# Kernel tuning notes

Hardware: AMD Instinct MI355X
Metric: run time of the kernel (lower is better)

## Reference

```python
import jax, jax.numpy as jnp
import numpy as np

B, S, D = 16, 4096, 64

def setup_inputs() -> dict:
    key = jax.random.key(0)
    kq, kk, kv = jax.random.split(key, 3)
    Q = jax.random.normal(kq, (B, S, D), dtype=jnp.float32)
    K = jax.random.normal(kk, (B, S, D), dtype=jnp.float32)
    V = jax.random.normal(kv, (B, S, D), dtype=jnp.float32)
    return {"Q": Q, "K": K, "V": V}

def reference(Q, K, V):
    d = K.shape[2]  # feature dim, matches K.transpose(1,2).size(1) in torch
    scale = 1.0 / jnp.sqrt(jnp.asarray(d, dtype=Q.dtype))
    # scores: [B, Sq, Sk]
    scores = jnp.einsum('bqd,bkd->bqk', Q, K) * scale
    attn = jax.nn.softmax(scores, axis=-1)
    # out: [B, Sq, Dv]
    return jnp.einsum('bqk,bkd->bqd', attn, V)
```

## Files before the change

kernel.cpp:

```cpp
#include <hip/hip_runtime.h>
#include <cstdint>


#define S_LEN 4096
#define HD    64
#define NSTG  64

typedef __bf16 bf16x8 __attribute__((ext_vector_type(8)));
typedef float  f32x16 __attribute__((ext_vector_type(16)));
typedef float  f32x2  __attribute__((ext_vector_type(2)));

__device__ __forceinline__ unsigned pack_bf16(float x, float y) {
  unsigned ux = __builtin_bit_cast(unsigned, x) + 0x8000u;
  unsigned uy = __builtin_bit_cast(unsigned, y) + 0x8000u;
  return (ux >> 16) | (uy & 0xffff0000u);
}
__device__ __forceinline__ unsigned cvt_pk(float lo, float hi) {
  unsigned d;
  asm("v_cvt_pk_bf16_f32 %0, %1, %2" : "=v"(d) : "v"(lo), "v"(hi));
  return d;
}
#define AS1 __attribute__((address_space(1)))
#define AS3 __attribute__((address_space(3)))
__device__ __forceinline__ void gld16(const void* g, void* l) {
  __builtin_amdgcn_global_load_lds((const AS1 void*)(uintptr_t)g,
                                   (AS3 void*)(uintptr_t)l, 16, 0, 0);
}

__global__ __launch_bounds__(256) void prep(const float* __restrict__ K,
                                            const float* __restrict__ V,
                                            uint16_t* __restrict__ Kw,
                                            uint16_t* __restrict__ Vw) {
  if (blockIdx.x < 2048) {
    const int t   = blockIdx.x * 256 + threadIdx.x;
    const int row = t >> 3;
    const int gs  = t & 7;
    const float* p = K + (size_t)row * 64 + ((gs ^ (row & 7)) << 3);
    float4 a = *(const float4*)p;
    float4 b = *(const float4*)(p + 4);
    uint4 o = {pack_bf16(a.x, a.y), pack_bf16(a.z, a.w),
               pack_bf16(b.x, b.y), pack_bf16(b.z, b.w)};
    *(uint4*)(Kw + (size_t)t * 8) = o;
    return;
  }
  const int blk = blockIdx.x - 2048;
  const int b = blk >> 6, st = blk & 63;
  const int t = threadIdx.x;
  __shared__ uint16_t Vb[64 * 72];
  const float* src = V + ((size_t)b * S_LEN + st * 64) * 64;
  const int k = t >> 2, dq = (t & 3) * 16;
  const float* p = src + k * 64 + dq;
  float4 x0 = *(const float4*)p,       x1 = *(const float4*)(p + 4);
  float4 x2 = *(const float4*)(p + 8), x3 = *(const float4*)(p + 12);
  unsigned* dst = (unsigned*)&Vb[k * 72 + dq];
  dst[0] = pack_bf16(x0.x, x0.y); dst[1] = pack_bf16(x0.z, x0.w);
  dst[2] = pack_bf16(x1.x, x1.y); dst[3] = pack_bf16(x1.z, x1.w);
  dst[4] = pack_bf16(x2.x, x2.y); dst[5] = pack_bf16(x2.z, x2.w);
  dst[6] = pack_bf16(x3.x, x3.y); dst[7] = pack_bf16(x3.z, x3.w);
  __syncthreads();
  uint16_t* out = Vw + ((size_t)b * 64 + st) * 4096;
#pragma unroll
  for (int j = 0; j < 2; ++j) {
    const int gi = t + j * 256;
    const int d = gi >> 3, gs = gi & 7;
    const int gsx = gs ^ (d & 7);
    const int kb = ((gsx >> 1) << 4) | ((gsx & 1) << 2);
    unsigned v0 = Vb[(kb + 0) * 72 + d], v1 = Vb[(kb + 1) * 72 + d];
    unsigned v2 = Vb[(kb + 2) * 72 + d], v3 = Vb[(kb + 3) * 72 + d];
    unsigned v4 = Vb[(kb + 8) * 72 + d], v5 = Vb[(kb + 9) * 72 + d];
    unsigned v6 = Vb[(kb + 10) * 72 + d], v7 = Vb[(kb + 11) * 72 + d];
    uint4 o = {v0 | (v1 << 16), v2 | (v3 << 16), v4 | (v5 << 16), v6 | (v7 << 16)};
    *(uint4*)(out + (size_t)gi * 8) = o;
  }
}

__global__ __launch_bounds__(256, 2) void attn_fwd(
    const float* __restrict__ Qg, float* __restrict__ Og,
    const uint16_t* __restrict__ Kw, const uint16_t* __restrict__ Vw) {
  const int bid   = blockIdx.x;
  const int batch = ((bid & 7) << 1) | (bid >> 8);
  const int q0    = ((bid >> 3) & 31) << 7;

  const int tid = threadIdx.x, wave = tid >> 6, lane = tid & 63;
  const int l32 = lane & 31, h = lane >> 5;
  const int wq = wave & 1, wk = wave >> 1;

  __shared__ __align__(16) unsigned char sm[32768];

  const uint16_t* Kb  = Kw + (size_t)batch * (S_LEN * HD);
  const uint16_t* Vtb = Vw + (size_t)batch * (S_LEN * HD);

  const float cs = 0.18033688011112042f;
  bf16x8 qf[2][4];
#pragma unroll
  for (int t = 0; t < 2; ++t) {
    const int qrow = q0 + t * 64 + wq * 32 + l32;
    const float* qp = Qg + ((size_t)batch * S_LEN + qrow) * 64;
#pragma unroll
    for (int dc = 0; dc < 4; ++dc) {
      const float* p = qp + dc * 16 + h * 8;
      float4 a = *(const float4*)p;
      float4 b = *(const float4*)(p + 4);
      uint4 uu = {pack_bf16(a.x * cs, a.y * cs), pack_bf16(a.z * cs, a.w * cs),
                  pack_bf16(b.x * cs, b.y * cs), pack_bf16(b.z * cs, b.w * cs)};
      qf[t][dc] = __builtin_bit_cast(bf16x8, uu);
    }
  }

  const int sw = l32 & 7;
  int aK[4], aV[4];
#pragma unroll
  for (int dc = 0; dc < 4; ++dc)
    aK[dc] = (wk * 32 + l32) * 128 + (((dc * 2 + h) ^ sw) << 4);
#pragma unroll
  for (int kc = 0; kc < 2; ++kc) {
    aV[kc * 2 + 0] = 16384 + l32 * 128 + (((wk * 4 + kc * 2 + h) ^ sw) << 4);
    aV[kc * 2 + 1] = 16384 + (32 + l32) * 128 + (((wk * 4 + kc * 2 + h) ^ sw) << 4);
  }

  auto stage = [&](int nxt, int nb) {
    const uint16_t* ks = Kb + (size_t)nxt * 4096 + wave * 1024 + lane * 8;
    const uint16_t* vs = Vtb + (size_t)nxt * 4096 + wave * 1024 + lane * 8;
    char* kd = (char*)sm + nb * 8192 + wave * 2048;
    char* vd = (char*)sm + 16384 + nb * 8192 + wave * 2048;
    gld16(ks, kd);
    gld16(ks + 512, kd + 1024);
    gld16(vs, vd);
    gld16(vs + 512, vd + 1024);
  };
  stage(0, 0);

  float zf;
  asm("v_mov_b32 %0, 0" : "=v"(zf));
  const f32x16 z16 = {zf, zf, zf, zf, zf, zf, zf, zf,
                      zf, zf, zf, zf, zf, zf, zf, zf};

  f32x16 acc00{}, acc01{}, acc10{}, acc11{};
  f32x2 rs0{}, rs1{};

  auto body = [&](int s, int cb) {
    __syncthreads();
    if (s + 1 < NSTG) stage(s + 1, cb ^ 1);
    const char* smc = (const char*)sm;
    f32x16 sc0, sc1;
    __builtin_amdgcn_s_setprio(1);
    {
      bf16x8 ka = *(const bf16x8*)(smc + cb * 8192 + aK[0]);
      sc0 = __builtin_amdgcn_mfma_f32_32x32x16_bf16(ka, qf[0][0], z16, 0, 0, 0);
      sc1 = __builtin_amdgcn_mfma_f32_32x32x16_bf16(ka, qf[1][0], z16, 0, 0, 0);
    }
#pragma unroll
    for (int dc = 1; dc < 4; ++dc) {
      bf16x8 ka = *(const bf16x8*)(smc + cb * 8192 + aK[dc]);
      sc0 = __builtin_amdgcn_mfma_f32_32x32x16_bf16(ka, qf[0][dc], sc0, 0, 0, 0);
      sc1 = __builtin_amdgcn_mfma_f32_32x32x16_bf16(ka, qf[1][dc], sc1, 0, 0, 0);
    }
    __builtin_amdgcn_s_setprio(0);
    bf16x8 v00 = *(const bf16x8*)(smc + cb * 8192 + aV[0]);
    bf16x8 v01 = *(const bf16x8*)(smc + cb * 8192 + aV[1]);
    bf16x8 v10 = *(const bf16x8*)(smc + cb * 8192 + aV[2]);
    bf16x8 v11 = *(const bf16x8*)(smc + cb * 8192 + aV[3]);
    unsigned w0[8];
#pragma unroll
    for (int j = 0; j < 8; ++j) {
      float a0 = __builtin_amdgcn_exp2f(sc0[2 * j]);
      float a1 = __builtin_amdgcn_exp2f(sc0[2 * j + 1]);
      f32x2 ta = {a0, a1};
      rs0 += ta;
      w0[j] = cvt_pk(a0, a1);
    }
    uint4 u00 = {w0[0], w0[1], w0[2], w0[3]};
    uint4 u01 = {w0[4], w0[5], w0[6], w0[7]};
    bf16x8 pa00 = __builtin_bit_cast(bf16x8, u00);
    bf16x8 pa01 = __builtin_bit_cast(bf16x8, u01);
    __builtin_amdgcn_s_setprio(1);
    acc00 = __builtin_amdgcn_mfma_f32_32x32x16_bf16(pa00, v00, acc00, 0, 0, 0);
    acc01 = __builtin_amdgcn_mfma_f32_32x32x16_bf16(pa00, v01, acc01, 0, 0, 0);
    acc00 = __builtin_amdgcn_mfma_f32_32x32x16_bf16(pa01, v10, acc00, 0, 0, 0);
    acc01 = __builtin_amdgcn_mfma_f32_32x32x16_bf16(pa01, v11, acc01, 0, 0, 0);
    __builtin_amdgcn_s_setprio(0);
    unsigned w1[8];
#pragma unroll
    for (int j = 0; j < 8; ++j) {
      float b0 = __builtin_amdgcn_exp2f(sc1[2 * j]);
      float b1 = __builtin_amdgcn_exp2f(sc1[2 * j + 1]);
      f32x2 tb = {b0, b1};
      rs1 += tb;
      w1[j] = cvt_pk(b0, b1);
    }
    uint4 u10 = {w1[0], w1[1], w1[2], w1[3]};
    uint4 u11 = {w1[4], w1[5], w1[6], w1[7]};
    bf16x8 pa10 = __builtin_bit_cast(bf16x8, u10);
    bf16x8 pa11 = __builtin_bit_cast(bf16x8, u11);
    __builtin_amdgcn_s_setprio(1);
    acc10 = __builtin_amdgcn_mfma_f32_32x32x16_bf16(pa10, v00, acc10, 0, 0, 0);
    acc11 = __builtin_amdgcn_mfma_f32_32x32x16_bf16(pa10, v01, acc11, 0, 0, 0);
    acc10 = __builtin_amdgcn_mfma_f32_32x32x16_bf16(pa11, v10, acc10, 0, 0, 0);
    acc11 = __builtin_amdgcn_mfma_f32_32x32x16_bf16(pa11, v11, acc11, 0, 0, 0);
    __builtin_amdgcn_s_setprio(0);
  };
  for (int it = 0; it < NSTG; it += 2) { body(it, 0); body(it + 1, 1); }

  float rsum0 = rs0[0] + rs0[1];
  float rsum1 = rs1[0] + rs1[1];
  rsum0 += __shfl_xor(rsum0, 32, 64);
  rsum1 += __shfl_xor(rsum1, 32, 64);
  float* exch = (float*)sm;
  const int ebase = wq * (33 * 64);
#pragma unroll
  for (int t = 0; t < 2; ++t) {
    const f32x16& a0 = t ? acc10 : acc00;
    const f32x16& a1 = t ? acc11 : acc01;
    const float rsum = t ? rsum1 : rsum0;
    __syncthreads();
    if (wk == 1) {
#pragma unroll
      for (int r = 0; r < 16; ++r) {
        exch[ebase + r * 64 + lane]        = a0[r];
        exch[ebase + (16 + r) * 64 + lane] = a1[r];
      }
      exch[ebase + 32 * 64 + lane] = rsum;
    }
    __syncthreads();
    if (wk == 0) {
      const float rt  = rsum + exch[ebase + 32 * 64 + lane];
      const float inv = __builtin_amdgcn_rcpf(rt);
      float* Ob = Og + ((size_t)batch * S_LEN + q0 + t * 64 + wq * 32) * 64;
#pragma unroll
      for (int r = 0; r < 16; ++r) {
        float o0 = a0[r] + exch[ebase + r * 64 + lane];
        float o1 = a1[r] + exch[ebase + (16 + r) * 64 + lane];
        const int qrl = (r & 3) + ((r >> 2) << 3) + (h << 2);
        const float iv = __shfl(inv, qrl, 64);
        float* op = Ob + (size_t)qrl * 64 + l32;
        op[0]  = o0 * iv;
        op[32] = o1 * iv;
      }
    }
  }
}

extern "C" void kernel_launch(void* const* d_in, const int* in_sizes, int n_in,
                              void* d_out, int out_size, void* d_ws, size_t ws_size,
                              hipStream_t stream) {
  const float* Q = (const float*)d_in[0];
  const float* K = (const float*)d_in[1];
  const float* V = (const float*)d_in[2];
  float* O = (float*)d_out;
  uint16_t* Kw = (uint16_t*)d_ws;
  uint16_t* Vw = Kw + (size_t)16 * S_LEN * HD;
  prep<<<dim3(3072), dim3(256), 0, stream>>>(K, V, Kw, Vw);
  attn_fwd<<<dim3(512), dim3(256), 0, stream>>>(Q, O, Kw, Vw);
}
```

Measured before the change: 163.4 us.

## Stage two K/V tiles per barrier with 64KB double-buffered shared memory

The main loop now prefetches two 64-key K/V stages per iteration into a larger 64KB shared buffer and computes both before the next barrier. This halves the number of __syncthreads calls and gives the async global-to-LDS loads more time to complete. The s_setprio hints around the MFMA blocks are also removed. The larger LDS footprint may limit how many blocks fit per CU, since launch bounds ask for 2 blocks.

```diff
diff --git a/kernel.cpp b/kernel.cpp
--- a/kernel.cpp
+++ b/kernel.cpp
@@ -85,7 +85,7 @@
   const int l32 = lane & 31, h = lane >> 5;
   const int wq = wave & 1, wk = wave >> 1;
 
-  __shared__ __align__(16) unsigned char sm[32768];
+  __shared__ __align__(16) unsigned char sm[65536];
 
   const uint16_t* Kb  = Kw + (size_t)batch * (S_LEN * HD);
   const uint16_t* Vtb = Vw + (size_t)batch * (S_LEN * HD);
@@ -114,21 +114,22 @@
     aK[dc] = (wk * 32 + l32) * 128 + (((dc * 2 + h) ^ sw) << 4);
 #pragma unroll
   for (int kc = 0; kc < 2; ++kc) {
-    aV[kc * 2 + 0] = 16384 + l32 * 128 + (((wk * 4 + kc * 2 + h) ^ sw) << 4);
-    aV[kc * 2 + 1] = 16384 + (32 + l32) * 128 + (((wk * 4 + kc * 2 + h) ^ sw) << 4);
-  }
-
-  auto stage = [&](int nxt, int nb) {
-    const uint16_t* ks = Kb + (size_t)nxt * 4096 + wave * 1024 + lane * 8;
-    const uint16_t* vs = Vtb + (size_t)nxt * 4096 + wave * 1024 + lane * 8;
-    char* kd = (char*)sm + nb * 8192 + wave * 2048;
-    char* vd = (char*)sm + 16384 + nb * 8192 + wave * 2048;
+    aV[kc * 2 + 0] = l32 * 128 + (((wk * 4 + kc * 2 + h) ^ sw) << 4);
+    aV[kc * 2 + 1] = (32 + l32) * 128 + (((wk * 4 + kc * 2 + h) ^ sw) << 4);
+  }
+
+  auto stage = [&](int s, int koff) {
+    const uint16_t* ks = Kb + (size_t)s * 4096 + wave * 1024 + lane * 8;
+    const uint16_t* vs = Vtb + (size_t)s * 4096 + wave * 1024 + lane * 8;
+    char* kd = (char*)sm + koff + wave * 2048;
+    char* vd = (char*)sm + 32768 + koff + wave * 2048;
     gld16(ks, kd);
     gld16(ks + 512, kd + 1024);
     gld16(vs, vd);
     gld16(vs + 512, vd + 1024);
   };
   stage(0, 0);
+  stage(1, 8192);
 
   float zf;
   asm("v_mov_b32 %0, 0" : "=v"(zf));
@@ -138,28 +139,24 @@
   f32x16 acc00{}, acc01{}, acc10{}, acc11{};
   f32x2 rs0{}, rs1{};
 
-  auto body = [&](int s, int cb) {
-    __syncthreads();
-    if (s + 1 < NSTG) stage(s + 1, cb ^ 1);
+  auto compute = [&](int koff) {
     const char* smc = (const char*)sm;
     f32x16 sc0, sc1;
-    __builtin_amdgcn_s_setprio(1);
     {
-      bf16x8 ka = *(const bf16x8*)(smc + cb * 8192 + aK[0]);
+      bf16x8 ka = *(const bf16x8*)(smc + koff + aK[0]);
       sc0 = __builtin_amdgcn_mfma_f32_32x32x16_bf16(ka, qf[0][0], z16, 0, 0, 0);
       sc1 = __builtin_amdgcn_mfma_f32_32x32x16_bf16(ka, qf[1][0], z16, 0, 0, 0);
     }
 #pragma unroll
     for (int dc = 1; dc < 4; ++dc) {
-      bf16x8 ka = *(const bf16x8*)(smc + cb * 8192 + aK[dc]);
+      bf16x8 ka = *(const bf16x8*)(smc + koff + aK[dc]);
       sc0 = __builtin_amdgcn_mfma_f32_32x32x16_bf16(ka, qf[0][dc], sc0, 0, 0, 0);
       sc1 = __builtin_amdgcn_mfma_f32_32x32x16_bf16(ka, qf[1][dc], sc1, 0, 0, 0);
     }
-    __builtin_amdgcn_s_setprio(0);
-    bf16x8 v00 = *(const bf16x8*)(smc + cb * 8192 + aV[0]);
-    bf16x8 v01 = *(const bf16x8*)(smc + cb * 8192 + aV[1]);
-    bf16x8 v10 = *(const bf16x8*)(smc + cb * 8192 + aV[2]);
-    bf16x8 v11 = *(const bf16x8*)(smc + cb * 8192 + aV[3]);
+    bf16x8 v00 = *(const bf16x8*)(smc + 32768 + koff + aV[0]);
+    bf16x8 v01 = *(const bf16x8*)(smc + 32768 + koff + aV[1]);
+    bf16x8 v10 = *(const bf16x8*)(smc + 32768 + koff + aV[2]);
+    bf16x8 v11 = *(const bf16x8*)(smc + 32768 + koff + aV[3]);
     unsigned w0[8];
 #pragma unroll
     for (int j = 0; j < 8; ++j) {
@@ -173,12 +170,10 @@
     uint4 u01 = {w0[4], w0[5], w0[6], w0[7]};
     bf16x8 pa00 = __builtin_bit_cast(bf16x8, u00);
     bf16x8 pa01 = __builtin_bit_cast(bf16x8, u01);
-    __builtin_amdgcn_s_setprio(1);
     acc00 = __builtin_amdgcn_mfma_f32_32x32x16_bf16(pa00, v00, acc00, 0, 0, 0);
     acc01 = __builtin_amdgcn_mfma_f32_32x32x16_bf16(pa00, v01, acc01, 0, 0, 0);
     acc00 = __builtin_amdgcn_mfma_f32_32x32x16_bf16(pa01, v10, acc00, 0, 0, 0);
     acc01 = __builtin_amdgcn_mfma_f32_32x32x16_bf16(pa01, v11, acc01, 0, 0, 0);
-    __builtin_amdgcn_s_setprio(0);
     unsigned w1[8];
 #pragma unroll
     for (int j = 0; j < 8; ++j) {
@@ -192,14 +187,22 @@
     uint4 u11 = {w1[4], w1[5], w1[6], w1[7]};
     bf16x8 pa10 = __builtin_bit_cast(bf16x8, u10);
     bf16x8 pa11 = __builtin_bit_cast(bf16x8, u11);
-    __builtin_amdgcn_s_setprio(1);
     acc10 = __builtin_amdgcn_mfma_f32_32x32x16_bf16(pa10, v00, acc10, 0, 0, 0);
     acc11 = __builtin_amdgcn_mfma_f32_32x32x16_bf16(pa10, v01, acc11, 0, 0, 0);
     acc10 = __builtin_amdgcn_mfma_f32_32x32x16_bf16(pa11, v10, acc10, 0, 0, 0);
     acc11 = __builtin_amdgcn_mfma_f32_32x32x16_bf16(pa11, v11, acc11, 0, 0, 0);
-    __builtin_amdgcn_s_setprio(0);
   };
-  for (int it = 0; it < NSTG; it += 2) { body(it, 0); body(it + 1, 1); }
+
+  for (int it = 0; it < NSTG; it += 2) {
+    __syncthreads();
+    const int p = (it >> 1) & 1;
+    if (it + 2 < NSTG) {
+      stage(it + 2, (p ^ 1) * 16384);
+      stage(it + 3, (p ^ 1) * 16384 + 8192);
+    }
+    compute(p * 16384);
+    compute(p * 16384 + 8192);
+  }
 
   float rsum0 = rs0[0] + rs0[1];
   float rsum1 = rs1[0] + rs1[1];
```

Measured after the change: 163.3 us. No clear change (-0.0%).

## Split key sequence across two blocks and combine partial outputs in a third kernel

Applied to the files above, without the earlier changes.

The attention kernel now launches twice as many blocks, each handling half of the key/value sequence for the same query tile. Each block writes unnormalized partial outputs and row sums, and a new combine kernel adds the two halves and normalizes. This targets under-occupancy from having only 512 blocks on a GPU with many CUs, at the cost of extra global traffic for partial outputs and an extra launch. It also drops the s_setprio hints and the explicit zero-init trick for the first score MFMA.

```diff
diff --git a/kernel.cpp b/kernel.cpp
--- a/kernel.cpp
+++ b/kernel.cpp
@@ -4,7 +4,7 @@
 
 #define S_LEN 4096
 #define HD    64
-#define NSTG  64
+#define NSTG  32
 
 typedef __bf16 bf16x8 __attribute__((ext_vector_type(8)));
 typedef float  f32x16 __attribute__((ext_vector_type(16)));
@@ -76,8 +76,10 @@
 
 __global__ __launch_bounds__(256, 2) void attn_fwd(
     const float* __restrict__ Qg, float* __restrict__ Og,
-    const uint16_t* __restrict__ Kw, const uint16_t* __restrict__ Vw) {
-  const int bid   = blockIdx.x;
+    const uint16_t* __restrict__ Kw, const uint16_t* __restrict__ Vw,
+    float* __restrict__ OpA, float* __restrict__ Rsum) {
+  const int bid   = blockIdx.x & 511;
+  const int kh    = blockIdx.x >> 9;
   const int batch = ((bid & 7) << 1) | (bid >> 8);
   const int q0    = ((bid >> 3) & 31) << 7;
 
@@ -87,8 +89,8 @@
 
   __shared__ __align__(16) unsigned char sm[32768];
 
-  const uint16_t* Kb  = Kw + (size_t)batch * (S_LEN * HD);
-  const uint16_t* Vtb = Vw + (size_t)batch * (S_LEN * HD);
+  const uint16_t* Kb  = Kw + (size_t)batch * (S_LEN * HD) + (size_t)kh * 131072;
+  const uint16_t* Vtb = Vw + (size_t)batch * (S_LEN * HD) + (size_t)kh * 131072;
 
   const float cs = 0.18033688011112042f;
   bf16x8 qf[2][4];
@@ -130,11 +132,6 @@
   };
   stage(0, 0);
 
-  float zf;
-  asm("v_mov_b32 %0, 0" : "=v"(zf));
-  const f32x16 z16 = {zf, zf, zf, zf, zf, zf, zf, zf,
-                      zf, zf, zf, zf, zf, zf, zf, zf};
-
   f32x16 acc00{}, acc01{}, acc10{}, acc11{};
   f32x2 rs0{}, rs1{};
 
@@ -142,20 +139,13 @@
     __syncthreads();
     if (s + 1 < NSTG) stage(s + 1, cb ^ 1);
     const char* smc = (const char*)sm;
-    f32x16 sc0, sc1;
-    __builtin_amdgcn_s_setprio(1);
-    {
-      bf16x8 ka = *(const bf16x8*)(smc + cb * 8192 + aK[0]);
-      sc0 = __builtin_amdgcn_mfma_f32_32x32x16_bf16(ka, qf[0][0], z16, 0, 0, 0);
-      sc1 = __builtin_amdgcn_mfma_f32_32x32x16_bf16(ka, qf[1][0], z16, 0, 0, 0);
-    }
-#pragma unroll
-    for (int dc = 1; dc < 4; ++dc) {
+    f32x16 sc0{}, sc1{};
+#pragma unroll
+    for (int dc = 0; dc < 4; ++dc) {
       bf16x8 ka = *(const bf16x8*)(smc + cb * 8192 + aK[dc]);
       sc0 = __builtin_amdgcn_mfma_f32_32x32x16_bf16(ka, qf[0][dc], sc0, 0, 0, 0);
       sc1 = __builtin_amdgcn_mfma_f32_32x32x16_bf16(ka, qf[1][dc], sc1, 0, 0, 0);
     }
-    __builtin_amdgcn_s_setprio(0);
     bf16x8 v00 = *(const bf16x8*)(smc + cb * 8192 + aV[0]);
     bf16x8 v01 = *(const bf16x8*)(smc + cb * 8192 + aV[1]);
     bf16x8 v10 = *(const bf16x8*)(smc + cb * 8192 + aV[2]);
@@ -173,12 +163,10 @@
     uint4 u01 = {w0[4], w0[5], w0[6], w0[7]};
     bf16x8 pa00 = __builtin_bit_cast(bf16x8, u00);
     bf16x8 pa01 = __builtin_bit_cast(bf16x8, u01);
-    __builtin_amdgcn_s_setprio(1);
     acc00 = __builtin_amdgcn_mfma_f32_32x32x16_bf16(pa00, v00, acc00, 0, 0, 0);
     acc01 = __builtin_amdgcn_mfma_f32_32x32x16_bf16(pa00, v01, acc01, 0, 0, 0);
     acc00 = __builtin_amdgcn_mfma_f32_32x32x16_bf16(pa01, v10, acc00, 0, 0, 0);
     acc01 = __builtin_amdgcn_mfma_f32_32x32x16_bf16(pa01, v11, acc01, 0, 0, 0);
-    __builtin_amdgcn_s_setprio(0);
     unsigned w1[8];
 #pragma unroll
     for (int j = 0; j < 8; ++j) {
@@ -192,12 +180,10 @@
     uint4 u11 = {w1[4], w1[5], w1[6], w1[7]};
     bf16x8 pa10 = __builtin_bit_cast(bf16x8, u10);
     bf16x8 pa11 = __builtin_bit_cast(bf16x8, u11);
-    __builtin_amdgcn_s_setprio(1);
     acc10 = __builtin_amdgcn_mfma_f32_32x32x16_bf16(pa10, v00, acc10, 0, 0, 0);
     acc11 = __builtin_amdgcn_mfma_f32_32x32x16_bf16(pa10, v01, acc11, 0, 0, 0);
     acc10 = __builtin_amdgcn_mfma_f32_32x32x16_bf16(pa11, v10, acc10, 0, 0, 0);
     acc11 = __builtin_amdgcn_mfma_f32_32x32x16_bf16(pa11, v11, acc11, 0, 0, 0);
-    __builtin_amdgcn_s_setprio(0);
   };
   for (int it = 0; it < NSTG; it += 2) { body(it, 0); body(it + 1, 1); }
 
@@ -207,6 +193,8 @@
   rsum1 += __shfl_xor(rsum1, 32, 64);
   float* exch = (float*)sm;
   const int ebase = wq * (33 * 64);
+  float* Opart = kh ? Og : OpA;
+  float* Rs = Rsum + (size_t)kh * (16 * S_LEN);
 #pragma unroll
   for (int t = 0; t < 2; ++t) {
     const f32x16& a0 = t ? acc10 : acc00;
@@ -223,21 +211,34 @@
     }
     __syncthreads();
     if (wk == 0) {
-      const float rt  = rsum + exch[ebase + 32 * 64 + lane];
-      const float inv = __builtin_amdgcn_rcpf(rt);
-      float* Ob = Og + ((size_t)batch * S_LEN + q0 + t * 64 + wq * 32) * 64;
+      const int qbase = q0 + t * 64 + wq * 32;
+      const float rt = rsum + exch[ebase + 32 * 64 + lane];
+      float* Ob = Opart + ((size_t)batch * S_LEN + qbase) * 64;
 #pragma unroll
       for (int r = 0; r < 16; ++r) {
         float o0 = a0[r] + exch[ebase + r * 64 + lane];
         float o1 = a1[r] + exch[ebase + (16 + r) * 64 + lane];
         const int qrl = (r & 3) + ((r >> 2) << 3) + (h << 2);
-        const float iv = __shfl(inv, qrl, 64);
         float* op = Ob + (size_t)qrl * 64 + l32;
-        op[0]  = o0 * iv;
-        op[32] = o1 * iv;
+        op[0]  = o0;
+        op[32] = o1;
       }
-    }
-  }
+      if (h == 0) Rs[(size_t)batch * S_LEN + qbase + l32] = rt;
+    }
+  }
+}
+
+__global__ __launch_bounds__(256) void combine(float* __restrict__ Og,
+                                               const float* __restrict__ OpA,
+                                               const float* __restrict__ R) {
+  const int idx = blockIdx.x * 256 + threadIdx.x;
+  const int row = idx >> 4;
+  float4 a = ((const float4*)OpA)[idx];
+  float4 b = ((const float4*)Og)[idx];
+  const float inv = __builtin_amdgcn_rcpf(R[row] + R[row + 16 * S_LEN]);
+  float4 o = {(a.x + b.x) * inv, (a.y + b.y) * inv,
+              (a.z + b.z) * inv, (a.w + b.w) * inv};
+  ((float4*)Og)[idx] = o;
 }
 
 extern "C" void kernel_launch(void* const* d_in, const int* in_sizes, int n_in,
@@ -249,6 +250,9 @@
   float* O = (float*)d_out;
   uint16_t* Kw = (uint16_t*)d_ws;
   uint16_t* Vw = Kw + (size_t)16 * S_LEN * HD;
+  float* OpA = (float*)(Vw + (size_t)16 * S_LEN * HD);
+  float* Rs  = OpA + (size_t)16 * S_LEN * HD;
   prep<<<dim3(3072), dim3(256), 0, stream>>>(K, V, Kw, Vw);
-  attn_fwd<<<dim3(512), dim3(256), 0, stream>>>(Q, O, Kw, Vw);
-}
+  attn_fwd<<<dim3(1024), dim3(256), 0, stream>>>(Q, O, Kw, Vw, OpA, Rs);
+  combine<<<dim3(4096), dim3(256), 0, stream>>>(O, OpA, Rs);
+}
```

Result: slower. 170.0 us (+4.1%).
